# Kernel tuning notes

Hardware: AMD Instinct MI355X
Metric: run time of the kernel (lower is better)

Reference implementation:

```python
import jax, jax.numpy as jnp
import numpy as np

B, N, C = 16, 3136, 384
H = W = 56
HEADS = 8
DH = C // HEADS
AG = 49          # agent_num
PS = 7           # pool size (sqrt(agent_num)); H % PS == 0 -> exact block mean
OUT = 1000
SCALE = DH ** -0.5


def setup_inputs() -> dict:
    key = jax.random.key(0)
    ks = jax.random.split(key, 16)
    f32 = jnp.float32

    def nrm(k, sh, s=0.02):
        return jax.random.normal(k, sh, f32) * s

    return dict(
        x=jax.random.normal(ks[0], (B, N, C), f32),
        Wq=nrm(ks[1], (C, C)),
        Wkv=nrm(ks[2], (C, 2 * C)),
        an_bias=nrm(ks[3], (HEADS, AG, H, W)),
        na_bias=nrm(ks[4], (HEADS, AG, H, W)),
        ah_bias=nrm(ks[5], (1, HEADS, AG, H, 1)),
        aw_bias=nrm(ks[6], (1, HEADS, AG, 1, W)),
        ha_bias=nrm(ks[7], (1, HEADS, H, 1, AG)),
        wa_bias=nrm(ks[8], (1, HEADS, 1, W, AG)),
        dwc_w=nrm(ks[9], (C, 1, 3, 3), 0.1),   # depthwise 3x3, groups=C (OIHW, I=1)
        dwc_b=jnp.zeros((C,), f32),
        Wproj=nrm(ks[10], (C, C)),
        bproj=jnp.zeros((C,), f32),
        ln_g=jnp.ones((C,), f32),
        ln_b=jnp.zeros((C,), f32),
        W1=nrm(ks[11], (C, 2 * C)),
        b1=jnp.zeros((2 * C,), f32),
        W2=nrm(ks[12], (2 * C, OUT)),
        b2=jnp.zeros((OUT,), f32),
    )


def _layernorm(x, g, b, eps=1e-5):
    m = x.mean(-1, keepdims=True)
    v = ((x - m) ** 2).mean(-1, keepdims=True)
    return (x - m) * jax.lax.rsqrt(v + eps) * g + b


def reference(x, Wq, Wkv, an_bias, na_bias, ah_bias, aw_bias, ha_bias, wa_bias,
              dwc_w, dwc_b, Wproj, bproj, ln_g, ln_b, W1, b1, W2, b2):
    q = x @ Wq                                  # (B,N,C)
    kv = x @ Wkv                                # (B,N,2C)  (sr_ratio=1 path)
    k, v = kv[..., :C], kv[..., C:]

    # agent tokens: AdaptiveAvgPool2d(7) on (B,C,56,56) == exact 8x8 block mean
    agent = q.reshape(B, PS, H // PS, PS, W // PS, C).mean((2, 4)).reshape(B, AG, C)

    qh = q.reshape(B, N, HEADS, DH).transpose(0, 2, 1, 3)      # (B,h,N,d)
    kh = k.reshape(B, N, HEADS, DH).transpose(0, 2, 1, 3)
    vh = v.reshape(B, N, HEADS, DH).transpose(0, 2, 1, 3)
    ah = agent.reshape(B, AG, HEADS, DH).transpose(0, 2, 1, 3)  # (B,h,AG,d)

    # stage 1: agent -> kv. bilinear interp to same size == identity (sr=1)
    pos_bias = an_bias.reshape(1, HEADS, AG, N) + (ah_bias + aw_bias).reshape(1, HEADS, AG, N)
    agent_attn = jax.nn.softmax(
        jnp.einsum('bhad,bhnd->bhan', ah * SCALE, kh) + pos_bias, axis=-1)
    agent_v = jnp.einsum('bhan,bhnd->bhad', agent_attn, vh)     # (B,h,AG,d)

    # stage 2: query -> agent
    agent_bias = (na_bias.reshape(1, HEADS, AG, N).transpose(0, 1, 3, 2)
                  + (ha_bias + wa_bias).reshape(1, HEADS, N, AG))
    q_attn = jax.nn.softmax(
        jnp.einsum('bhnd,bhad->bhna', qh * SCALE, ah) + agent_bias, axis=-1)
    out = jnp.einsum('bhna,bhad->bhnd', q_attn, agent_v)
    out = out.transpose(0, 2, 1, 3).reshape(B, N, C)

    # depthwise conv residual on v (sr=1 -> no interpolation)
    v_img = v.reshape(B, H, W, C).transpose(0, 3, 1, 2)          # (B,C,H,W)
    dwc = jax.lax.conv_general_dilated(
        v_img, dwc_w, (1, 1), 'SAME', feature_group_count=C,
        dimension_numbers=('NCHW', 'OIHW', 'NCHW')) + dwc_b[None, :, None, None]
    out = out + dwc.transpose(0, 2, 3, 1).reshape(B, N, C)

    out = out @ Wproj + bproj
    pooled = out.mean(axis=1)                   # adaptive_avg_pool2d to 1x1
    h1 = _layernorm(pooled, ln_g, ln_b)
    h1 = jax.nn.gelu(h1 @ W1 + b1, approximate=False)
    return h1 @ W2 + b2                         # (B, OUT)
```

## Files before the change

kernel.cpp:

```cpp
#include <hip/hip_runtime.h>
#include <hip/hip_bf16.h>
#include <math.h>

#define BB 16
#define NN 3136
#define CC 384
#define HDS 8
#define DHH 48
#define AGG 49
#define HI 56
#define WI 56
#define OUTD 1000
#define SCALE_F 0.14433756729740643f
#define QKVC 1152

typedef __attribute__((ext_vector_type(8))) short short8;
typedef __attribute__((ext_vector_type(4))) float f32x4;

__device__ __forceinline__ float bf2f(unsigned short u) {
  union { unsigned u32; float f; } x;
  x.u32 = ((unsigned)u) << 16;
  return x.f;
}
__device__ __forceinline__ unsigned short f2bf(float f) {
  union { float f; unsigned u; } x;
  x.f = f;
  unsigned u = x.u;
  unsigned r = (u + 0x7fffu + ((u >> 16) & 1u)) >> 16;
  return (unsigned short)r;
}

__device__ __forceinline__ size_t xp_off(int gb, int ks, int j, int lane) {
  return ((((size_t)gb * 12 + ks) * 4 + j) * 64 + lane) * 8;
}
__device__ __forceinline__ size_t wp_off(int blk, int ks, int i, int lane) {
  return ((((size_t)blk * 12 + ks) * 4 + i) * 64 + lane) * 8;
}
__device__ __forceinline__ size_t vtp_off(int bh, int chunk, int half, int ntd, int lane) {
  return ((((size_t)bh * 49 + chunk) * 2 + half) * 3 + ntd) * 512 + lane * 8;
}

__global__ __launch_bounds__(256) void pack_x(const float* __restrict__ x,
                                              unsigned short* __restrict__ xp) {
  __shared__ unsigned short xlds[64 * 200];
  int gb = blockIdx.x;
  int tid = threadIdx.x;
  int lane = tid & 63, wv = tid >> 6;
  int lo = lane & 15, g = lane >> 4;
  int tok0 = gb * 64;

  for (int kh = 0; kh < 2; kh++) {
    if (kh) __syncthreads();
#pragma unroll
    for (int it = 0; it < 12; it++) {
      int idx = tid + it * 256;
      int tok = idx / 48, k4 = idx % 48;
      float4 f = *(const float4*)&x[(size_t)(tok0 + tok) * 384 + kh * 192 + k4 * 4];
      uint2 o;
      o.x = (unsigned)f2bf(f.x) | ((unsigned)f2bf(f.y) << 16);
      o.y = (unsigned)f2bf(f.z) | ((unsigned)f2bf(f.w) << 16);
      *(uint2*)&xlds[tok * 200 + k4 * 4] = o;
    }
    __syncthreads();
    for (int p = wv; p < 24; p += 4) {
      int ks = p >> 2, j = p & 3;
      uint4 v = *(const uint4*)&xlds[(j * 16 + lo) * 200 + ks * 32 + g * 8];
      *(uint4*)&xp[xp_off(gb, kh * 6 + ks, j, lane)] = v;
    }
  }
}

__global__ __launch_bounds__(256) void pack_w(const float* __restrict__ Wq,
                                              const float* __restrict__ Wkv,
                                              unsigned short* __restrict__ wp) {
  __shared__ unsigned short wlds[64 * 392];
  int blk = blockIdx.x;
  int col0 = blk * 64;
  const float* src;
  int ncol, nloc;
  if (col0 < 384) { src = Wq; ncol = 384; nloc = col0; }
  else            { src = Wkv; ncol = 768; nloc = col0 - 384; }
  int tid = threadIdx.x;
  int lane = tid & 63, wv = tid >> 6;
  int lo = lane & 15, g = lane >> 4;

#pragma unroll
  for (int it = 0; it < 96; it++) {
    int idx = tid + it * 256;
    int k = idx >> 6, col = idx & 63;
    wlds[col * 392 + k] = f2bf(src[(size_t)k * ncol + nloc + col]);
  }
  __syncthreads();
  for (int p = wv; p < 48; p += 4) {
    int ks = p >> 2, i = p & 3;
    uint4 v = *(const uint4*)&wlds[(i * 16 + lo) * 392 + ks * 32 + g * 8];
    *(uint4*)&wp[wp_off(blk, ks, i, lane)] = v;
  }
}

__global__ __launch_bounds__(256, 2) void gemm_v4(const unsigned short* __restrict__ xp,
                                                  const unsigned short* __restrict__ wp,
                                                  unsigned short* __restrict__ Y) {
  const int tid = threadIdx.x;
  const int lane = tid & 63;
  const int wave = tid >> 6;
  const int lo = lane & 15, g = lane >> 4;
  const int wt2 = wave & 1;
  const int wn2 = wave >> 1;

  int wg = blockIdx.x;
  int xcd = wg & 7, idx8 = wg >> 3;
  const int sq = 220, sr = 4;
  int l = (xcd < sr ? xcd * (sq + 1) : sr * (sq + 1) + (xcd - sr) * sq) + idx8;
  int bx = l % 9, by = l / 9;

  const int gbb = by * 4 + wt2 * 2;
  const unsigned short* wbase = wp + wp_off(bx * 2 + wn2, 0, 0, lane);
  const unsigned short* xbase0 = xp + xp_off(gbb + 0, 0, 0, lane);
  const unsigned short* xbase1 = xp + xp_off(gbb + 1, 0, 0, lane);

  f32x4 acc[4][8];
#pragma unroll
  for (int i = 0; i < 4; i++)
#pragma unroll
    for (int jj = 0; jj < 8; jj++) acc[i][jj] = (f32x4)0.f;

  short8 wfA[4], xfA[8], wfB[4], xfB[8];

  auto loadF = [&](short8* wf, short8* xf, int ks) {
    const unsigned short* wptr = wbase + (size_t)ks * 2048;
#pragma unroll
    for (int i = 0; i < 4; i++) wf[i] = *(const short8*)(wptr + i * 512);
    const unsigned short* x0 = xbase0 + (size_t)ks * 2048;
    const unsigned short* x1 = xbase1 + (size_t)ks * 2048;
#pragma unroll
    for (int j = 0; j < 4; j++) {
      xf[j] = *(const short8*)(x0 + j * 512);
      xf[4 + j] = *(const short8*)(x1 + j * 512);
    }
  };
  auto mfmaF = [&](short8* wf, short8* xf) {
    __builtin_amdgcn_s_setprio(1);
#pragma unroll
    for (int i = 0; i < 4; i++)
#pragma unroll
      for (int jj = 0; jj < 8; jj++)
        acc[i][jj] = __builtin_amdgcn_mfma_f32_16x16x32_bf16(wf[i], xf[jj], acc[i][jj], 0, 0, 0);
    __builtin_amdgcn_s_setprio(0);
  };

  loadF(wfA, xfA, 0);
#pragma unroll
  for (int kp = 0; kp < 6; kp++) {
    loadF(wfB, xfB, 2 * kp + 1);
    mfmaF(wfA, xfA);
    if (kp < 5) loadF(wfA, xfA, 2 * kp + 2);
    mfmaF(wfB, xfB);
  }

#pragma unroll
  for (int jj = 0; jj < 8; jj++) {
    int token = (gbb + (jj >> 2)) * 64 + (jj & 3) * 16 + lo;
#pragma unroll
    for (int i = 0; i < 4; i++) {
      int ncol = bx * 128 + wn2 * 64 + i * 16 + g * 4;
      uint2 o;
      o.x = (unsigned)f2bf(acc[i][jj][0]) | ((unsigned)f2bf(acc[i][jj][1]) << 16);
      o.y = (unsigned)f2bf(acc[i][jj][2]) | ((unsigned)f2bf(acc[i][jj][3]) << 16);
      *(uint2*)&Y[(size_t)token * QKVC + ncol] = o;
    }
  }
}

__global__ __launch_bounds__(256) void make_cbias2(
    const float* __restrict__ na, const float* __restrict__ ha,
    const float* __restrict__ wa, const float* __restrict__ an,
    const float* __restrict__ ah, const float* __restrict__ aw,
    unsigned short* __restrict__ cb1t, unsigned short* __restrict__ cb2t) {
  int blk = blockIdx.x;
  int h = blk / 49, nc = blk % 49;
  int a = threadIdx.x & 63, sub = threadIdx.x >> 6;
  int ac = a < AGG ? a : AGG - 1;
  bool va = a < AGG;
  size_t hab = (size_t)h * AGG + ac;
#pragma unroll
  for (int i = 0; i < 16; i++) {
    int n = nc * 64 + i * 4 + sub;
    int r = n / WI, c = n % WI;
    float v1 = na[hab * NN + n] + ha[(h * HI + r) * AGG + ac] + wa[(h * WI + c) * AGG + ac];
    float v2 = an[hab * NN + n] + ah[hab * HI + r] + aw[hab * WI + c];
    size_t ob = ((size_t)h * NN + n) * 52;
    if (a < 52) {
      cb1t[ob + a] = va ? f2bf(v1) : (unsigned short)0;
      cb2t[ob + a] = va ? f2bf(v2) : (unsigned short)0;
    }
  }
}

#define VSTR 396
__global__ __launch_bounds__(256) void pack_vt(const unsigned short* __restrict__ qkv,
                                               unsigned short* __restrict__ vtp) {
  __shared__ unsigned short vlds[64 * VSTR];
  int blk = blockIdx.x;
  int b = blk / 49, chunk = blk % 49;
  int tid = threadIdx.x, lane = tid & 63, wv = tid >> 6;
  int lo = lane & 15, g = lane >> 4;

#pragma unroll
  for (int it = 0; it < 12; it++) {
    int idx = tid + it * 256;
    int t = idx / 48, d8 = idx % 48;
    short8 v = *(const short8*)&qkv[((size_t)b * NN + chunk * 64 + t) * QKVC + 768 + d8 * 8];
    *(uint2*)&vlds[t * VSTR + d8 * 8] = ((uint2*)&v)[0];
    *(uint2*)&vlds[t * VSTR + d8 * 8 + 4] = ((uint2*)&v)[1];
  }
  __syncthreads();
  int bh8 = b * 8;
#pragma unroll
  for (int p = 0; p < 12; p++) {
    int fid = wv * 12 + p;
    int h = fid / 6, rem = fid % 6, half = rem / 3, ntd = rem % 3;
    unsigned short tmp[8];
#pragma unroll
    for (int e = 0; e < 8; e++)
      tmp[e] = vlds[(half * 32 + g * 8 + e) * VSTR + h * 48 + ntd * 16 + lo];
    *(uint4*)&vtp[vtp_off(bh8 + h, chunk, half, ntd, lane)] = *(uint4*)tmp;
  }
}

__global__ __launch_bounds__(384) void pool_agent(const unsigned short* __restrict__ qkv,
                                                  unsigned short* __restrict__ agbf) {
  int blk = blockIdx.x;
  int b = blk / AGG, a = blk % AGG;
  int p1 = a / 7, p2 = a % 7;
  int c = threadIdx.x;
  float s = 0.f;
#pragma unroll
  for (int i = 0; i < 8; i++)
#pragma unroll
    for (int j = 0; j < 8; j++) {
      int n = (p1 * 8 + i) * WI + (p2 * 8 + j);
      s += bf2f(qkv[((size_t)b * NN + n) * QKVC + c]);
    }
  agbf[(size_t)blk * CC + c] = f2bf(s * (1.f / 64.f));
}

__global__ __launch_bounds__(256) void agent_attn_v5(
    const unsigned short* __restrict__ qkv, const unsigned short* __restrict__ agbf,
    const unsigned short* __restrict__ cb2t, const unsigned short* __restrict__ vtp,
    float* __restrict__ lpart, float* __restrict__ avpart) {
  int z = blockIdx.x;
  int s = z & 3;
  int h = (z >> 2) & 7;
  int b = z >> 5;
  int tid = threadIdx.x, lane = tid & 63, wv = tid >> 6;
  int lo = lane & 15, g = lane >> 4;
  int slot = s * 4 + wv;
  int cstart = (slot == 0) ? 0 : 3 * slot + 1;
  int ccount = (slot == 0) ? 4 : 3;
  int bh = b * 8 + h;

  __shared__ __align__(16) unsigned short pT[4][64 * 72];
  __shared__ float ldsAV[AGG * 48];
  __shared__ float ldsL[AGG];
  for (int i = tid; i < AGG * 48; i += 256) ldsAV[i] = 0.f;
  if (tid < AGG) ldsL[tid] = 0.f;
  __syncthreads();

  short8 af0[4], af1[4];
#pragma unroll
  for (int mt = 0; mt < 4; mt++) {
    int a = mt * 16 + lo;
    int ac = a < AGG ? a : AGG - 1;
    const unsigned short* p = agbf + ((size_t)b * AGG + ac) * CC + h * 48;
    af0[mt] = *(const short8*)(p + g * 8);
    if (g < 2) af1[mt] = *(const short8*)(p + 32 + g * 8);
    else { short8 zz = {0, 0, 0, 0, 0, 0, 0, 0}; af1[mt] = zz; }
  }

  f32x4 acc2[4][3];
#pragma unroll
  for (int mt = 0; mt < 4; mt++)
#pragma unroll
    for (int ntd = 0; ntd < 3; ntd++) acc2[mt][ntd] = (f32x4)0.f;
  float lacc[4][4];
#pragma unroll
  for (int mt = 0; mt < 4; mt++)
#pragma unroll
    for (int r = 0; r < 4; r++) lacc[mt][r] = 0.f;

  for (int ci = 0; ci < ccount; ci++) {
    int chunk = cstart + ci;
    int nb = chunk * 64;

    short8 kf0[4], kf1[4];
#pragma unroll
    for (int nt = 0; nt < 4; nt++) {
      const unsigned short* kp = qkv + ((size_t)b * NN + nb + nt * 16 + lo) * QKVC + 384 + h * 48;
      kf0[nt] = *(const short8*)(kp + g * 8);
      if (g < 2) kf1[nt] = *(const short8*)(kp + 32 + g * 8);
      else { short8 zz = {0, 0, 0, 0, 0, 0, 0, 0}; kf1[nt] = zz; }
    }
    ushort4 cbv[4][4];
#pragma unroll
    for (int mt = 0; mt < 4; mt++)
#pragma unroll
      for (int nt = 0; nt < 4; nt++)
        cbv[mt][nt] = *(const ushort4*)&cb2t[((size_t)h * NN + nb + nt * 16 + lo) * 52 + mt * 16 + g * 4];
    short8 vb0[3], vb1[3];
#pragma unroll
    for (int ntd = 0; ntd < 3; ntd++) {
      vb0[ntd] = *(const short8*)&vtp[vtp_off(bh, chunk, 0, ntd, lane)];
      vb1[ntd] = *(const short8*)&vtp[vtp_off(bh, chunk, 1, ntd, lane)];
    }

    f32x4 acc[4][4];
#pragma unroll
    for (int mt = 0; mt < 4; mt++)
#pragma unroll
      for (int nt = 0; nt < 4; nt++) acc[mt][nt] = (f32x4)0.f;
#pragma unroll
    for (int mt = 0; mt < 4; mt++)
#pragma unroll
      for (int nt = 0; nt < 4; nt++) {
        acc[mt][nt] = __builtin_amdgcn_mfma_f32_16x16x32_bf16(af0[mt], kf0[nt], acc[mt][nt], 0, 0, 0);
        acc[mt][nt] = __builtin_amdgcn_mfma_f32_16x16x32_bf16(af1[mt], kf1[nt], acc[mt][nt], 0, 0, 0);
      }

#pragma unroll
    for (int mt = 0; mt < 4; mt++)
#pragma unroll
      for (int nt = 0; nt < 4; nt++) {
        unsigned short cb4[4] = {cbv[mt][nt].x, cbv[mt][nt].y, cbv[mt][nt].z, cbv[mt][nt].w};
#pragma unroll
        for (int r = 0; r < 4; r++) {
          int a = mt * 16 + g * 4 + r;
          float e = 0.f;
          if (a < AGG) e = __expf(acc[mt][nt][r] * SCALE_F + bf2f(cb4[r]));
          acc[mt][nt][r] = e;
        }
      }
#pragma unroll
    for (int mt = 0; mt < 4; mt++)
#pragma unroll
      for (int r = 0; r < 4; r++)
        lacc[mt][r] += acc[mt][0][r] + acc[mt][1][r] + acc[mt][2][r] + acc[mt][3][r];
#pragma unroll
    for (int mt = 0; mt < 4; mt++)
#pragma unroll
      for (int nt = 0; nt < 4; nt++)
#pragma unroll
        for (int r = 0; r < 4; r++) {
          int a = mt * 16 + g * 4 + r;
          int t = nt * 16 + lo;
          pT[wv][a * 72 + t] = f2bf(acc[mt][nt][r]);
        }

    short8 pa0[4], pa1[4];
#pragma unroll
    for (int mt = 0; mt < 4; mt++) {
      const unsigned short* p = &pT[wv][(mt * 16 + lo) * 72 + g * 8];
      pa0[mt] = *(const short8*)p;
      pa1[mt] = *(const short8*)(p + 32);
    }
#pragma unroll
    for (int mt = 0; mt < 4; mt++)
#pragma unroll
      for (int ntd = 0; ntd < 3; ntd++) {
        acc2[mt][ntd] = __builtin_amdgcn_mfma_f32_16x16x32_bf16(pa0[mt], vb0[ntd], acc2[mt][ntd], 0, 0, 0);
        acc2[mt][ntd] = __builtin_amdgcn_mfma_f32_16x16x32_bf16(pa1[mt], vb1[ntd], acc2[mt][ntd], 0, 0, 0);
      }
  }

#pragma unroll
  for (int mt = 0; mt < 4; mt++)
#pragma unroll
    for (int r = 0; r < 4; r++) {
      float v = lacc[mt][r];
      v += __shfl_xor(v, 1); v += __shfl_xor(v, 2);
      v += __shfl_xor(v, 4); v += __shfl_xor(v, 8);
      if (lo == 0) {
        int a = mt * 16 + g * 4 + r;
        if (a < AGG) atomicAdd(&ldsL[a], v);
      }
    }
#pragma unroll
  for (int mt = 0; mt < 4; mt++)
#pragma unroll
    for (int ntd = 0; ntd < 3; ntd++)
#pragma unroll
      for (int r = 0; r < 4; r++) {
        int a = mt * 16 + g * 4 + r;
        if (a < AGG) atomicAdd(&ldsAV[a * 48 + ntd * 16 + lo], acc2[mt][ntd][r]);
      }
  __syncthreads();
  size_t pbase = (size_t)bh * 4 + s;
  for (int i = tid; i < AGG * 48; i += 256) avpart[pbase * 2352 + i] = ldsAV[i];
  if (tid < AGG) lpart[pbase * AGG + tid] = ldsL[tid];
}

__global__ __launch_bounds__(256) void av_normalize3(const float* __restrict__ lpart,
                                                     const float* __restrict__ avpart,
                                                     unsigned short* __restrict__ avtp) {
  int bh = blockIdx.x;
  int tid = threadIdx.x;
  __shared__ float linv[AGG];
  if (tid < AGG) {
    float l = 0.f;
#pragma unroll
    for (int s = 0; s < 4; s++) l += lpart[((size_t)bh * 4 + s) * AGG + tid];
    linv[tid] = 1.f / l;
  }
  __syncthreads();
  for (int idx = tid; idx < 48 * 64; idx += 256) {
    int d = idx >> 6, a = idx & 63;
    unsigned short o = 0;
    if (a < AGG) {
      float v = 0.f;
#pragma unroll
      for (int s = 0; s < 4; s++) v += avpart[((size_t)bh * 4 + s) * 2352 + a * 48 + d];
      o = f2bf(v * linv[a]);
    }
    avtp[(size_t)bh * 3072 + d * 64 + a] = o;
  }
}

__global__ __launch_bounds__(256) void q_attn_v5(
    const unsigned short* __restrict__ qkv, const unsigned short* __restrict__ agbf,
    const unsigned short* __restrict__ avtp, const unsigned short* __restrict__ cb1t,
    float* __restrict__ opart) {
  int z = blockIdx.x;
  int s = z & 3;
  int h = (z >> 2) & 7;
  int b = z >> 5;
  int tid = threadIdx.x, lane = tid & 63, wv = tid >> 6;
  int lo = lane & 15, g = lane >> 4;
  int slot = s * 4 + wv;
  int cstart = (slot == 0) ? 0 : 3 * slot + 1;
  int ccount = (slot == 0) ? 4 : 3;
  int bh = b * 8 + h;

  __shared__ __align__(16) unsigned short pT[4][64 * 72];
  __shared__ float ldsO[48];
  if (tid < 48) ldsO[tid] = 0.f;
  __syncthreads();

  short8 af0[4], af1[4];
#pragma unroll
  for (int mt = 0; mt < 4; mt++) {
    int a = mt * 16 + lo;
    int ac = a < AGG ? a : AGG - 1;
    const unsigned short* p = agbf + ((size_t)b * AGG + ac) * CC + h * 48;
    af0[mt] = *(const short8*)(p + g * 8);
    if (g < 2) af1[mt] = *(const short8*)(p + 32 + g * 8);
    else { short8 zz = {0, 0, 0, 0, 0, 0, 0, 0}; af1[mt] = zz; }
  }
  short8 vf0[3], vf1[3];
#pragma unroll
  for (int mtd = 0; mtd < 3; mtd++) {
    size_t base = ((size_t)bh * 48 + mtd * 16 + lo) * 64;
    vf0[mtd] = *(const short8*)&avtp[base + g * 8];
    vf1[mtd] = *(const short8*)&avtp[base + 32 + g * 8];
  }

  f32x4 acc2[3][4];
#pragma unroll
  for (int mtd = 0; mtd < 3; mtd++)
#pragma unroll
    for (int nt = 0; nt < 4; nt++) acc2[mtd][nt] = (f32x4)0.f;

  for (int ci = 0; ci < ccount; ci++) {
    int nb = (cstart + ci) * 64;

    short8 qf0[4], qf1[4];
#pragma unroll
    for (int nt = 0; nt < 4; nt++) {
      const unsigned short* qp = qkv + ((size_t)b * NN + nb + nt * 16 + lo) * QKVC + h * 48;
      qf0[nt] = *(const short8*)(qp + g * 8);
      if (g < 2) qf1[nt] = *(const short8*)(qp + 32 + g * 8);
      else { short8 zz = {0, 0, 0, 0, 0, 0, 0, 0}; qf1[nt] = zz; }
    }
    ushort4 cbv[4][4];
#pragma unroll
    for (int mt = 0; mt < 4; mt++)
#pragma unroll
      for (int nt = 0; nt < 4; nt++)
        cbv[mt][nt] = *(const ushort4*)&cb1t[((size_t)h * NN + nb + nt * 16 + lo) * 52 + mt * 16 + g * 4];

    f32x4 acc[4][4];
#pragma unroll
    for (int mt = 0; mt < 4; mt++)
#pragma unroll
      for (int nt = 0; nt < 4; nt++) acc[mt][nt] = (f32x4)0.f;
#pragma unroll
    for (int mt = 0; mt < 4; mt++)
#pragma unroll
      for (int nt = 0; nt < 4; nt++) {
        acc[mt][nt] = __builtin_amdgcn_mfma_f32_16x16x32_bf16(af0[mt], qf0[nt], acc[mt][nt], 0, 0, 0);
        acc[mt][nt] = __builtin_amdgcn_mfma_f32_16x16x32_bf16(af1[mt], qf1[nt], acc[mt][nt], 0, 0, 0);
      }

#pragma unroll
    for (int nt = 0; nt < 4; nt++) {
      float lsum = 0.f;
#pragma unroll
      for (int mt = 0; mt < 4; mt++) {
        unsigned short cb4[4] = {cbv[mt][nt].x, cbv[mt][nt].y, cbv[mt][nt].z, cbv[mt][nt].w};
#pragma unroll
        for (int r = 0; r < 4; r++) {
          int a = mt * 16 + g * 4 + r;
          float e = 0.f;
          if (a < AGG) e = __expf(acc[mt][nt][r] * SCALE_F + bf2f(cb4[r]));
          acc[mt][nt][r] = e;
          lsum += e;
        }
      }
      lsum += __shfl_xor(lsum, 16);
      lsum += __shfl_xor(lsum, 32);
      float inv = 1.f / lsum;
      int t = nt * 16 + lo;
#pragma unroll
      for (int mt = 0; mt < 4; mt++)
#pragma unroll
        for (int rp = 0; rp < 2; rp++) {
          unsigned u0 = f2bf(acc[mt][nt][rp * 2] * inv);
          unsigned u1 = f2bf(acc[mt][nt][rp * 2 + 1] * inv);
          int a = mt * 16 + g * 4 + rp * 2;
          *(unsigned*)&pT[wv][t * 72 + a] = u0 | (u1 << 16);
        }
    }

    short8 pf0[4], pf1[4];
#pragma unroll
    for (int nt = 0; nt < 4; nt++) {
      const unsigned short* p = &pT[wv][(nt * 16 + lo) * 72 + g * 8];
      pf0[nt] = *(const short8*)p;
      pf1[nt] = *(const short8*)(p + 32);
    }
#pragma unroll
    for (int mtd = 0; mtd < 3; mtd++)
#pragma unroll
      for (int nt = 0; nt < 4; nt++) {
        acc2[mtd][nt] = __builtin_amdgcn_mfma_f32_16x16x32_bf16(vf0[mtd], pf0[nt], acc2[mtd][nt], 0, 0, 0);
        acc2[mtd][nt] = __builtin_amdgcn_mfma_f32_16x16x32_bf16(vf1[mtd], pf1[nt], acc2[mtd][nt], 0, 0, 0);
      }
  }

#pragma unroll
  for (int mtd = 0; mtd < 3; mtd++)
#pragma unroll
    for (int r = 0; r < 4; r++) {
      float v = acc2[mtd][0][r] + acc2[mtd][1][r] + acc2[mtd][2][r] + acc2[mtd][3][r];
      v += __shfl_xor(v, 1); v += __shfl_xor(v, 2);
      v += __shfl_xor(v, 4); v += __shfl_xor(v, 8);
      if (lo == 0) atomicAdd(&ldsO[mtd * 16 + g * 4 + r], v);
    }
  __syncthreads();
  if (tid < 48) opart[((size_t)bh * 4 + s) * 48 + tid] = ldsO[tid];
}

__global__ __launch_bounds__(384) void dwc_rows(const unsigned short* __restrict__ qkv,
                                                float* __restrict__ rowsum,
                                                float* __restrict__ edge0,
                                                float* __restrict__ edge1) {
  int z = blockIdx.x;
  int b = z / HI, r = z % HI;
  int c = threadIdx.x;
  const unsigned short* base = qkv + ((size_t)b * NN + (size_t)r * WI) * QKVC + 768 + c;
  float s = 0.f, e0 = 0.f, e1 = 0.f;
  for (int w = 0; w < WI; w++) {
    float v = bf2f(base[(size_t)w * QKVC]);
    s += v;
    if (w == 0) e0 = v;
    if (w == WI - 1) e1 = v;
  }
  rowsum[(size_t)z * CC + c] = s;
  edge0[(size_t)z * CC + c] = e0;
  edge1[(size_t)z * CC + c] = e1;
}

__global__ __launch_bounds__(384) void dwc_combine1(const float* __restrict__ rowsum,
                                                    const float* __restrict__ edge0,
                                                    const float* __restrict__ edge1,
                                                    float* __restrict__ dpart,
                                                    float* __restrict__ dedge) {
  int z = blockIdx.x;
  int b = z / 7, rc = z % 7;
  int c = threadIdx.x;
  float T = 0.f, C0 = 0.f, C55 = 0.f;
#pragma unroll
  for (int rr = 0; rr < 8; rr++) {
    int r = rc * 8 + rr;
    size_t idx = ((size_t)(b * HI + r)) * CC + c;
    float rs = rowsum[idx], a0 = edge0[idx], a1 = edge1[idx];
    T += rs; C0 += a0; C55 += a1;
    if (r == 0) {
      dedge[((size_t)b * 6 + 0) * CC + c] = rs;
      dedge[((size_t)b * 6 + 1) * CC + c] = a0;
      dedge[((size_t)b * 6 + 2) * CC + c] = a1;
    }
    if (r == HI - 1) {
      dedge[((size_t)b * 6 + 3) * CC + c] = rs;
      dedge[((size_t)b * 6 + 4) * CC + c] = a0;
      dedge[((size_t)b * 6 + 5) * CC + c] = a1;
    }
  }
  size_t pb = ((size_t)(b * 7 + rc) * 3) * CC + c;
  dpart[pb] = T;
  dpart[pb + CC] = C0;
  dpart[pb + 2 * CC] = C55;
}

__global__ __launch_bounds__(384) void head_pre(const float* __restrict__ dpart,
                                                const float* __restrict__ dedge,
                                                const float* __restrict__ opart,
                                                const float* __restrict__ w,
                                                const float* __restrict__ dwc_b,
                                                float* __restrict__ pre) {
  int b = blockIdx.x;
  int k = threadIdx.x;
  float T = 0.f, C0 = 0.f, C55 = 0.f;
#pragma unroll
  for (int rc = 0; rc < 7; rc++) {
    size_t pb = ((size_t)(b * 7 + rc) * 3) * CC + k;
    T += dpart[pb];
    C0 += dpart[pb + CC];
    C55 += dpart[pb + 2 * CC];
  }
  float R0 = dedge[((size_t)b * 6 + 0) * CC + k];
  float v00 = dedge[((size_t)b * 6 + 1) * CC + k];
  float v0W = dedge[((size_t)b * 6 + 2) * CC + k];
  float R55 = dedge[((size_t)b * 6 + 3) * CC + k];
  float vH0 = dedge[((size_t)b * 6 + 4) * CC + k];
  float vHW = dedge[((size_t)b * 6 + 5) * CC + k];
  float dwcsum = 0.f;
#pragma unroll
  for (int i = 0; i < 3; i++) {
    int di = i - 1;
#pragma unroll
    for (int j = 0; j < 3; j++) {
      int dj = j - 1;
      float S = T;
      if (di == 1) S -= R0; else if (di == -1) S -= R55;
      if (dj == 1) S -= C0; else if (dj == -1) S -= C55;
      if (di != 0 && dj != 0)
        S += (di == 1) ? ((dj == 1) ? v00 : v0W) : ((dj == 1) ? vH0 : vHW);
      dwcsum += w[k * 9 + i * 3 + j] * S;
    }
  }
  int hh = k / 48, dd = k % 48;
  size_t obase = ((size_t)(b * 8 + hh) * 4) * 48;
  float attn = 0.f;
#pragma unroll
  for (int s = 0; s < 4; s++) attn += opart[obase + s * 48 + dd];
  pre[(size_t)b * CC + k] = (dwcsum + attn) * (1.f / (float)NN) + dwc_b[k];
}

__global__ __launch_bounds__(256) void head_proj_part(
    const float* __restrict__ pre, const float* __restrict__ Wproj,
    float* __restrict__ pjpart) {
  int w = blockIdx.x * 4 + (threadIdx.x >> 6);
  int lane = threadIdx.x & 63;
  int b = w / 36, rem = w % 36;
  int oc = rem / 6, kc = rem % 6;
  int o = oc * 64 + lane;
  const float* pb = pre + (size_t)b * CC + kc * 64;
  const float* wp2 = Wproj + (size_t)(kc * 64) * CC + o;
  float s = 0.f;
#pragma unroll 16
  for (int k = 0; k < 64; k++) s += pb[k] * wp2[(size_t)k * CC];
  pjpart[((size_t)(b * 6 + kc)) * CC + o] = s;
}

__global__ __launch_bounds__(384) void head_ln6(const float* __restrict__ pjpart,
                                                const float* __restrict__ bproj,
                                                const float* __restrict__ ln_g,
                                                const float* __restrict__ ln_b,
                                                float* __restrict__ h0) {
  int b = blockIdx.x;
  int tid = threadIdx.x;
  __shared__ float red[8];
  float v = bproj[tid];
#pragma unroll
  for (int kc = 0; kc < 6; kc++) v += pjpart[((size_t)(b * 6 + kc)) * CC + tid];
  float m;
  {
    float s = v;
#pragma unroll
    for (int o = 32; o > 0; o >>= 1) s += __shfl_down(s, o);
    if ((tid & 63) == 0) red[tid >> 6] = s;
    __syncthreads();
    if (tid == 0) {
      float t = 0.f;
      for (int i = 0; i < 6; i++) t += red[i];
      red[6] = t * (1.f / (float)CC);
    }
    __syncthreads();
    m = red[6];
  }
  float dv = v - m;
  __syncthreads();
  float var;
  {
    float s = dv * dv;
#pragma unroll
    for (int o = 32; o > 0; o >>= 1) s += __shfl_down(s, o);
    if ((tid & 63) == 0) red[tid >> 6] = s;
    __syncthreads();
    if (tid == 0) {
      float t = 0.f;
      for (int i = 0; i < 6; i++) t += red[i];
      red[7] = t * (1.f / (float)CC);
    }
    __syncthreads();
    var = red[7];
  }
  h0[(size_t)b * CC + tid] = dv * rsqrtf(var + 1e-5f) * ln_g[tid] + ln_b[tid];
}

__global__ __launch_bounds__(256) void head_mlp1_part(
    const float* __restrict__ h0, const float* __restrict__ W1,
    float* __restrict__ h1part) {
  int w = blockIdx.x * 4 + (threadIdx.x >> 6);
  int lane = threadIdx.x & 63;
  int b = w / 72, rem = w % 72;
  int oc = rem / 6, kc = rem % 6;
  int o = oc * 64 + lane;
  const float* hb = h0 + (size_t)b * CC + kc * 64;
  const float* wp2 = W1 + (size_t)(kc * 64) * (2 * CC) + o;
  float s = 0.f;
#pragma unroll 16
  for (int k = 0; k < 64; k++) s += hb[k] * wp2[(size_t)k * (2 * CC)];
  h1part[((size_t)(b * 6 + kc)) * (2 * CC) + o] = s;
}

__global__ __launch_bounds__(256) void head_mlp1_red(const float* __restrict__ h1part,
                                                     const float* __restrict__ b1,
                                                     float* __restrict__ h1) {
  int b = blockIdx.x;
  for (int o = threadIdx.x; o < 2 * CC; o += 256) {
    float s = b1[o];
#pragma unroll
    for (int kc = 0; kc < 6; kc++) s += h1part[((size_t)(b * 6 + kc)) * (2 * CC) + o];
    h1[(size_t)b * (2 * CC) + o] = 0.5f * s * (1.f + erff(s * 0.70710678118654752f));
  }
}

__global__ __launch_bounds__(256) void head_mlp2_part(
    const float* __restrict__ h1, const float* __restrict__ W2,
    float* __restrict__ o2part) {
  int w = blockIdx.x * 4 + (threadIdx.x >> 6);
  int lane = threadIdx.x & 63;
  int b = w / 192, rem = w % 192;
  int oc = rem / 12, kc = rem % 12;
  int o = oc * 64 + lane;
  int ocl = o < OUTD ? o : OUTD - 1;
  const float* hb = h1 + (size_t)b * (2 * CC) + kc * 64;
  const float* wp2 = W2 + (size_t)(kc * 64) * OUTD + ocl;
  float s = 0.f;
#pragma unroll 16
  for (int k = 0; k < 64; k++) s += hb[k] * wp2[(size_t)k * OUTD];
  o2part[((size_t)(b * 12 + kc)) * 1024 + o] = s;
}

__global__ __launch_bounds__(256) void head_out(const float* __restrict__ o2part,
                                                const float* __restrict__ b2,
                                                float* __restrict__ out) {
  int b = blockIdx.x;
  for (int o = threadIdx.x; o < OUTD; o += 256) {
    float s = b2[o];
#pragma unroll
    for (int kc = 0; kc < 12; kc++) s += o2part[((size_t)(b * 12 + kc)) * 1024 + o];
    out[(size_t)b * OUTD + o] = s;
  }
}

extern "C" void kernel_launch(void* const* d_in, const int* in_sizes, int n_in,
                              void* d_out, int out_size, void* d_ws,
                              size_t ws_size, hipStream_t stream) {
  const float* x = (const float*)d_in[0];
  const float* Wq = (const float*)d_in[1];
  const float* Wkv = (const float*)d_in[2];
  const float* an_bias = (const float*)d_in[3];
  const float* na_bias = (const float*)d_in[4];
  const float* ah_bias = (const float*)d_in[5];
  const float* aw_bias = (const float*)d_in[6];
  const float* ha_bias = (const float*)d_in[7];
  const float* wa_bias = (const float*)d_in[8];
  const float* dwc_w = (const float*)d_in[9];
  const float* dwc_b = (const float*)d_in[10];
  const float* Wproj = (const float*)d_in[11];
  const float* bproj = (const float*)d_in[12];
  const float* ln_g = (const float*)d_in[13];
  const float* ln_b = (const float*)d_in[14];
  const float* W1 = (const float*)d_in[15];
  const float* b1 = (const float*)d_in[16];
  const float* W2 = (const float*)d_in[17];
  const float* b2 = (const float*)d_in[18];
  float* out = (float*)d_out;

  const size_t M = (size_t)BB * NN;
  char* wsp = (char*)d_ws;
  unsigned short* xp = (unsigned short*)wsp;
  unsigned short* vtp = xp;
  wsp += M * CC * 2;
  unsigned short* wpb = (unsigned short*)wsp;   wsp += (size_t)QKVC * CC * 2;
  unsigned short* qkv = (unsigned short*)wsp;   wsp += M * QKVC * 2;
  unsigned short* agbf = (unsigned short*)wsp;  wsp += (size_t)784 * CC * 2;
  unsigned short* cb1t = (unsigned short*)wsp;  wsp += (size_t)HDS * NN * 52 * 2;
  unsigned short* cb2t = (unsigned short*)wsp;  wsp += (size_t)HDS * NN * 52 * 2;
  float* lpart = (float*)wsp;                   wsp += (size_t)128 * 4 * AGG * 4;
  float* avpart = (float*)wsp;                  wsp += (size_t)128 * 4 * 2352 * 4;
  unsigned short* avtp = (unsigned short*)wsp;  wsp += (size_t)128 * 3072 * 2;
  float* opart = (float*)wsp;                   wsp += (size_t)128 * 4 * 48 * 4;
  float* rowsum = (float*)wsp;                  wsp += (size_t)BB * HI * CC * 4;
  float* edge0 = (float*)wsp;                   wsp += (size_t)BB * HI * CC * 4;
  float* edge1 = (float*)wsp;                   wsp += (size_t)BB * HI * CC * 4;
  float* dpart = (float*)wsp;                   wsp += (size_t)BB * 7 * 3 * CC * 4;
  float* dedge = (float*)wsp;                   wsp += (size_t)BB * 6 * CC * 4;
  float* pre = (float*)wsp;                     wsp += (size_t)BB * CC * 4;
  float* pjpart = (float*)wsp;                  wsp += (size_t)BB * 6 * CC * 4;
  float* h0b = (float*)wsp;                     wsp += (size_t)BB * CC * 4;
  float* h1part = (float*)wsp;                  wsp += (size_t)BB * 6 * 2 * CC * 4;
  float* h1b = (float*)wsp;                     wsp += (size_t)BB * 2 * CC * 4;
  float* o2part = (float*)wsp;                  wsp += (size_t)BB * 12 * 1024 * 4;

  dim3 blk256(256);
  hipLaunchKernelGGL(pack_x, dim3(784), blk256, 0, stream, x, xp);
  hipLaunchKernelGGL(pack_w, dim3(18), blk256, 0, stream, Wq, Wkv, wpb);
  hipLaunchKernelGGL(make_cbias2, dim3(HDS * 49), blk256, 0, stream, na_bias,
                     ha_bias, wa_bias, an_bias, ah_bias, aw_bias, cb1t, cb2t);
  hipLaunchKernelGGL(gemm_v4, dim3(1764), blk256, 0, stream, xp, wpb, qkv);
  hipLaunchKernelGGL(pack_vt, dim3(BB * 49), blk256, 0, stream, qkv, vtp);
  hipLaunchKernelGGL(pool_agent, dim3(BB * AGG), dim3(384), 0, stream, qkv, agbf);
  hipLaunchKernelGGL(agent_attn_v5, dim3(BB * HDS * 4), blk256, 0, stream,
                     qkv, agbf, cb2t, vtp, lpart, avpart);
  hipLaunchKernelGGL(av_normalize3, dim3(BB * HDS), blk256, 0, stream, lpart,
                     avpart, avtp);
  hipLaunchKernelGGL(q_attn_v5, dim3(BB * HDS * 4), blk256, 0, stream, qkv,
                     agbf, avtp, cb1t, opart);
  hipLaunchKernelGGL(dwc_rows, dim3(BB * HI), dim3(384), 0, stream, qkv, rowsum,
                     edge0, edge1);
  hipLaunchKernelGGL(dwc_combine1, dim3(BB * 7), dim3(384), 0, stream, rowsum,
                     edge0, edge1, dpart, dedge);
  hipLaunchKernelGGL(head_pre, dim3(BB), dim3(384), 0, stream, dpart, dedge,
                     opart, dwc_w, dwc_b, pre);
  hipLaunchKernelGGL(head_proj_part, dim3(144), blk256, 0, stream, pre, Wproj, pjpart);
  hipLaunchKernelGGL(head_ln6, dim3(BB), dim3(384), 0, stream, pjpart, bproj,
                     ln_g, ln_b, h0b);
  hipLaunchKernelGGL(head_mlp1_part, dim3(288), blk256, 0, stream, h0b, W1, h1part);
  hipLaunchKernelGGL(head_mlp1_red, dim3(BB), blk256, 0, stream, h1part, b1, h1b);
  hipLaunchKernelGGL(head_mlp2_part, dim3(768), blk256, 0, stream, h1b, W2, o2part);
  hipLaunchKernelGGL(head_out, dim3(BB), blk256, 0, stream, o2part, b2, out);
}
```

Before: 268.4 us.

## Double-buffer K/Q fragment loads and write per-wave partials instead of LDS atomics

Both attention kernels now prefetch the next chunk's K (or Q) fragments into a second register set while the current chunk is computed, which hides global load latency. The shared-memory atomic reductions and their barriers are removed. Each wave now writes its own partial sums to global memory (16 slots per batch-head instead of 4), and the normalize and head kernels sum over 16 partials. This costs more registers, 4x larger partial buffers and more global traffic in the reduction kernels.

```diff
diff --git a/kernel.cpp b/kernel.cpp
--- a/kernel.cpp
+++ b/kernel.cpp
@@ -245,7 +245,7 @@
   agbf[(size_t)blk * CC + c] = f2bf(s * (1.f / 64.f));
 }
 
-__global__ __launch_bounds__(256) void agent_attn_v5(
+__global__ __launch_bounds__(256) void agent_attn_v7(
     const unsigned short* __restrict__ qkv, const unsigned short* __restrict__ agbf,
     const unsigned short* __restrict__ cb2t, const unsigned short* __restrict__ vtp,
     float* __restrict__ lpart, float* __restrict__ avpart) {
@@ -261,11 +261,6 @@
   int bh = b * 8 + h;
 
   __shared__ __align__(16) unsigned short pT[4][64 * 72];
-  __shared__ float ldsAV[AGG * 48];
-  __shared__ float ldsL[AGG];
-  for (int i = tid; i < AGG * 48; i += 256) ldsAV[i] = 0.f;
-  if (tid < AGG) ldsL[tid] = 0.f;
-  __syncthreads();
 
   short8 af0[4], af1[4];
 #pragma unroll
@@ -289,18 +284,19 @@
 #pragma unroll
     for (int r = 0; r < 4; r++) lacc[mt][r] = 0.f;
 
-  for (int ci = 0; ci < ccount; ci++) {
-    int chunk = cstart + ci;
+  auto loadK = [&](short8* k0, short8* k1, int chunk) {
     int nb = chunk * 64;
-
-    short8 kf0[4], kf1[4];
 #pragma unroll
     for (int nt = 0; nt < 4; nt++) {
       const unsigned short* kp = qkv + ((size_t)b * NN + nb + nt * 16 + lo) * QKVC + 384 + h * 48;
-      kf0[nt] = *(const short8*)(kp + g * 8);
-      if (g < 2) kf1[nt] = *(const short8*)(kp + 32 + g * 8);
-      else { short8 zz = {0, 0, 0, 0, 0, 0, 0, 0}; kf1[nt] = zz; }
-    }
+      k0[nt] = *(const short8*)(kp + g * 8);
+      if (g < 2) k1[nt] = *(const short8*)(kp + 32 + g * 8);
+      else { short8 zz = {0, 0, 0, 0, 0, 0, 0, 0}; k1[nt] = zz; }
+    }
+  };
+
+  auto body = [&](short8* k0, short8* k1, int chunk) {
+    int nb = chunk * 64;
     ushort4 cbv[4][4];
 #pragma unroll
     for (int mt = 0; mt < 4; mt++)
@@ -323,8 +319,8 @@
     for (int mt = 0; mt < 4; mt++)
 #pragma unroll
       for (int nt = 0; nt < 4; nt++) {
-        acc[mt][nt] = __builtin_amdgcn_mfma_f32_16x16x32_bf16(af0[mt], kf0[nt], acc[mt][nt], 0, 0, 0);
-        acc[mt][nt] = __builtin_amdgcn_mfma_f32_16x16x32_bf16(af1[mt], kf1[nt], acc[mt][nt], 0, 0, 0);
+        acc[mt][nt] = __builtin_amdgcn_mfma_f32_16x16x32_bf16(af0[mt], k0[nt], acc[mt][nt], 0, 0, 0);
+        acc[mt][nt] = __builtin_amdgcn_mfma_f32_16x16x32_bf16(af1[mt], k1[nt], acc[mt][nt], 0, 0, 0);
       }
 
 #pragma unroll
@@ -370,8 +366,21 @@
         acc2[mt][ntd] = __builtin_amdgcn_mfma_f32_16x16x32_bf16(pa0[mt], vb0[ntd], acc2[mt][ntd], 0, 0, 0);
         acc2[mt][ntd] = __builtin_amdgcn_mfma_f32_16x16x32_bf16(pa1[mt], vb1[ntd], acc2[mt][ntd], 0, 0, 0);
       }
-  }
-
+  };
+
+  short8 kA0[4], kA1[4], kB0[4], kB1[4];
+  loadK(kA0, kA1, cstart);
+  int ci = 0;
+  while (true) {
+    if (ci + 1 < ccount) loadK(kB0, kB1, cstart + ci + 1);
+    body(kA0, kA1, cstart + ci);
+    if (++ci >= ccount) break;
+    if (ci + 1 < ccount) loadK(kA0, kA1, cstart + ci + 1);
+    body(kB0, kB1, cstart + ci);
+    if (++ci >= ccount) break;
+  }
+
+  size_t pbase = (size_t)bh * 16 + slot;
 #pragma unroll
   for (int mt = 0; mt < 4; mt++)
 #pragma unroll
@@ -379,10 +388,8 @@
       float v = lacc[mt][r];
       v += __shfl_xor(v, 1); v += __shfl_xor(v, 2);
       v += __shfl_xor(v, 4); v += __shfl_xor(v, 8);
-      if (lo == 0) {
-        int a = mt * 16 + g * 4 + r;
-        if (a < AGG) atomicAdd(&ldsL[a], v);
-      }
+      int a = mt * 16 + g * 4 + r;
+      if (lo == 0 && a < AGG) lpart[pbase * AGG + a] = v;
     }
 #pragma unroll
   for (int mt = 0; mt < 4; mt++)
@@ -391,12 +398,9 @@
 #pragma unroll
       for (int r = 0; r < 4; r++) {
         int a = mt * 16 + g * 4 + r;
-        if (a < AGG) atomicAdd(&ldsAV[a * 48 + ntd * 16 + lo], acc2[mt][ntd][r]);
+        if (a < AGG)
+          avpart[pbase * 2352 + a * 48 + ntd * 16 + lo] = acc2[mt][ntd][r];
       }
-  __syncthreads();
-  size_t pbase = (size_t)bh * 4 + s;
-  for (int i = tid; i < AGG * 48; i += 256) avpart[pbase * 2352 + i] = ldsAV[i];
-  if (tid < AGG) lpart[pbase * AGG + tid] = ldsL[tid];
 }
 
 __global__ __launch_bounds__(256) void av_normalize3(const float* __restrict__ lpart,
@@ -408,7 +412,7 @@
   if (tid < AGG) {
     float l = 0.f;
 #pragma unroll
-    for (int s = 0; s < 4; s++) l += lpart[((size_t)bh * 4 + s) * AGG + tid];
+    for (int s = 0; s < 16; s++) l += lpart[((size_t)bh * 16 + s) * AGG + tid];
     linv[tid] = 1.f / l;
   }
   __syncthreads();
@@ -418,14 +422,14 @@
     if (a < AGG) {
       float v = 0.f;
 #pragma unroll
-      for (int s = 0; s < 4; s++) v += avpart[((size_t)bh * 4 + s) * 2352 + a * 48 + d];
+      for (int s = 0; s < 16; s++) v += avpart[((size_t)bh * 16 + s) * 2352 + a * 48 + d];
       o = f2bf(v * linv[a]);
     }
     avtp[(size_t)bh * 3072 + d * 64 + a] = o;
   }
 }
 
-__global__ __launch_bounds__(256) void q_attn_v5(
+__global__ __launch_bounds__(256) void q_attn_v7(
     const unsigned short* __restrict__ qkv, const unsigned short* __restrict__ agbf,
     const unsigned short* __restrict__ avtp, const unsigned short* __restrict__ cb1t,
     float* __restrict__ opart) {
@@ -441,9 +445,6 @@
   int bh = b * 8 + h;
 
   __shared__ __align__(16) unsigned short pT[4][64 * 72];
-  __shared__ float ldsO[48];
-  if (tid < 48) ldsO[tid] = 0.f;
-  __syncthreads();
 
   short8 af0[4], af1[4];
 #pragma unroll
@@ -469,17 +470,19 @@
 #pragma unroll
     for (int nt = 0; nt < 4; nt++) acc2[mtd][nt] = (f32x4)0.f;
 
-  for (int ci = 0; ci < ccount; ci++) {
-    int nb = (cstart + ci) * 64;
-
-    short8 qf0[4], qf1[4];
+  auto loadQ = [&](short8* q0, short8* q1, int chunk) {
+    int nb = chunk * 64;
 #pragma unroll
     for (int nt = 0; nt < 4; nt++) {
       const unsigned short* qp = qkv + ((size_t)b * NN + nb + nt * 16 + lo) * QKVC + h * 48;
-      qf0[nt] = *(const short8*)(qp + g * 8);
-      if (g < 2) qf1[nt] = *(const short8*)(qp + 32 + g * 8);
-      else { short8 zz = {0, 0, 0, 0, 0, 0, 0, 0}; qf1[nt] = zz; }
-    }
+      q0[nt] = *(const short8*)(qp + g * 8);
+      if (g < 2) q1[nt] = *(const short8*)(qp + 32 + g * 8);
+      else { short8 zz = {0, 0, 0, 0, 0, 0, 0, 0}; q1[nt] = zz; }
+    }
+  };
+
+  auto body = [&](short8* q0, short8* q1, int chunk) {
+    int nb = chunk * 64;
     ushort4 cbv[4][4];
 #pragma unroll
     for (int mt = 0; mt < 4; mt++)
@@ -496,8 +499,8 @@
     for (int mt = 0; mt < 4; mt++)
 #pragma unroll
       for (int nt = 0; nt < 4; nt++) {
-        acc[mt][nt] = __builtin_amdgcn_mfma_f32_16x16x32_bf16(af0[mt], qf0[nt], acc[mt][nt], 0, 0, 0);
-        acc[mt][nt] = __builtin_amdgcn_mfma_f32_16x16x32_bf16(af1[mt], qf1[nt], acc[mt][nt], 0, 0, 0);
+        acc[mt][nt] = __builtin_amdgcn_mfma_f32_16x16x32_bf16(af0[mt], q0[nt], acc[mt][nt], 0, 0, 0);
+        acc[mt][nt] = __builtin_amdgcn_mfma_f32_16x16x32_bf16(af1[mt], q1[nt], acc[mt][nt], 0, 0, 0);
       }
 
 #pragma unroll
@@ -544,8 +547,21 @@
         acc2[mtd][nt] = __builtin_amdgcn_mfma_f32_16x16x32_bf16(vf0[mtd], pf0[nt], acc2[mtd][nt], 0, 0, 0);
         acc2[mtd][nt] = __builtin_amdgcn_mfma_f32_16x16x32_bf16(vf1[mtd], pf1[nt], acc2[mtd][nt], 0, 0, 0);
       }
-  }
-
+  };
+
+  short8 qA0[4], qA1[4], qB0[4], qB1[4];
+  loadQ(qA0, qA1, cstart);
+  int ci = 0;
+  while (true) {
+    if (ci + 1 < ccount) loadQ(qB0, qB1, cstart + ci + 1);
+    body(qA0, qA1, cstart + ci);
+    if (++ci >= ccount) break;
+    if (ci + 1 < ccount) loadQ(qA0, qA1, cstart + ci + 1);
+    body(qB0, qB1, cstart + ci);
+    if (++ci >= ccount) break;
+  }
+
+  size_t pbase = (size_t)bh * 16 + slot;
 #pragma unroll
   for (int mtd = 0; mtd < 3; mtd++)
 #pragma unroll
@@ -553,10 +569,8 @@
       float v = acc2[mtd][0][r] + acc2[mtd][1][r] + acc2[mtd][2][r] + acc2[mtd][3][r];
       v += __shfl_xor(v, 1); v += __shfl_xor(v, 2);
       v += __shfl_xor(v, 4); v += __shfl_xor(v, 8);
-      if (lo == 0) atomicAdd(&ldsO[mtd * 16 + g * 4 + r], v);
-    }
-  __syncthreads();
-  if (tid < 48) opart[((size_t)bh * 4 + s) * 48 + tid] = ldsO[tid];
+      if (lo == 0) opart[pbase * 48 + mtd * 16 + g * 4 + r] = v;
+    }
 }
 
 __global__ __launch_bounds__(384) void dwc_rows(const unsigned short* __restrict__ qkv,
@@ -649,10 +663,10 @@
     }
   }
   int hh = k / 48, dd = k % 48;
-  size_t obase = ((size_t)(b * 8 + hh) * 4) * 48;
+  size_t obase = ((size_t)(b * 8 + hh) * 16) * 48;
   float attn = 0.f;
 #pragma unroll
-  for (int s = 0; s < 4; s++) attn += opart[obase + s * 48 + dd];
+  for (int s = 0; s < 16; s++) attn += opart[obase + s * 48 + dd];
   pre[(size_t)b * CC + k] = (dwcsum + attn) * (1.f / (float)NN) + dwc_b[k];
 }
 
@@ -809,10 +823,10 @@
   unsigned short* agbf = (unsigned short*)wsp;  wsp += (size_t)784 * CC * 2;
   unsigned short* cb1t = (unsigned short*)wsp;  wsp += (size_t)HDS * NN * 52 * 2;
   unsigned short* cb2t = (unsigned short*)wsp;  wsp += (size_t)HDS * NN * 52 * 2;
-  float* lpart = (float*)wsp;                   wsp += (size_t)128 * 4 * AGG * 4;
-  float* avpart = (float*)wsp;                  wsp += (size_t)128 * 4 * 2352 * 4;
+  float* lpart = (float*)wsp;                   wsp += (size_t)128 * 16 * AGG * 4;
+  float* avpart = (float*)wsp;                  wsp += (size_t)128 * 16 * 2352 * 4;
   unsigned short* avtp = (unsigned short*)wsp;  wsp += (size_t)128 * 3072 * 2;
-  float* opart = (float*)wsp;                   wsp += (size_t)128 * 4 * 48 * 4;
+  float* opart = (float*)wsp;                   wsp += (size_t)128 * 16 * 48 * 4;
   float* rowsum = (float*)wsp;                  wsp += (size_t)BB * HI * CC * 4;
   float* edge0 = (float*)wsp;                   wsp += (size_t)BB * HI * CC * 4;
   float* edge1 = (float*)wsp;                   wsp += (size_t)BB * HI * CC * 4;
@@ -833,11 +847,11 @@
   hipLaunchKernelGGL(gemm_v4, dim3(1764), blk256, 0, stream, xp, wpb, qkv);
   hipLaunchKernelGGL(pack_vt, dim3(BB * 49), blk256, 0, stream, qkv, vtp);
   hipLaunchKernelGGL(pool_agent, dim3(BB * AGG), dim3(384), 0, stream, qkv, agbf);
-  hipLaunchKernelGGL(agent_attn_v5, dim3(BB * HDS * 4), blk256, 0, stream,
+  hipLaunchKernelGGL(agent_attn_v7, dim3(BB * HDS * 4), blk256, 0, stream,
                      qkv, agbf, cb2t, vtp, lpart, avpart);
   hipLaunchKernelGGL(av_normalize3, dim3(BB * HDS), blk256, 0, stream, lpart,
                      avpart, avtp);
-  hipLaunchKernelGGL(q_attn_v5, dim3(BB * HDS * 4), blk256, 0, stream, qkv,
+  hipLaunchKernelGGL(q_attn_v7, dim3(BB * HDS * 4), blk256, 0, stream, qkv,
                      agbf, avtp, cb1t, opart);
   hipLaunchKernelGGL(dwc_rows, dim3(BB * HI), dim3(384), 0, stream, qkv, rowsum,
                      edge0, edge1);
```

After: 273.3 us. About the same (+1.8%).

## Sum query-agent attention over tokens before multiplying by agent values

Applied to the files above, without the earlier changes.

Because only the token-mean of the attention output is needed, the query-side kernel now accumulates per-agent softmax probability sums instead of running a second MFMA against agent_v. The agent_v product moves into head_pre as a small 49-term dot product using fp32 agent_v, and the bf16 transposed agent_v packing is dropped. This removes the LDS staging, the bf16 conversion and the second matmul from the hot kernel. In exchange, head_pre does a little more work and reads more partials (16 slots per head).

```diff
diff --git a/kernel.cpp b/kernel.cpp
--- a/kernel.cpp
+++ b/kernel.cpp
@@ -399,9 +399,9 @@
   if (tid < AGG) lpart[pbase * AGG + tid] = ldsL[tid];
 }
 
-__global__ __launch_bounds__(256) void av_normalize3(const float* __restrict__ lpart,
+__global__ __launch_bounds__(256) void av_normalize4(const float* __restrict__ lpart,
                                                      const float* __restrict__ avpart,
-                                                     unsigned short* __restrict__ avtp) {
+                                                     float* __restrict__ av) {
   int bh = blockIdx.x;
   int tid = threadIdx.x;
   __shared__ float linv[AGG];
@@ -412,23 +412,18 @@
     linv[tid] = 1.f / l;
   }
   __syncthreads();
-  for (int idx = tid; idx < 48 * 64; idx += 256) {
-    int d = idx >> 6, a = idx & 63;
-    unsigned short o = 0;
-    if (a < AGG) {
-      float v = 0.f;
-#pragma unroll
-      for (int s = 0; s < 4; s++) v += avpart[((size_t)bh * 4 + s) * 2352 + a * 48 + d];
-      o = f2bf(v * linv[a]);
-    }
-    avtp[(size_t)bh * 3072 + d * 64 + a] = o;
-  }
-}
-
-__global__ __launch_bounds__(256) void q_attn_v5(
+  for (int idx = tid; idx < AGG * 48; idx += 256) {
+    int a = idx / 48;
+    float v = 0.f;
+#pragma unroll
+    for (int s = 0; s < 4; s++) v += avpart[((size_t)bh * 4 + s) * 2352 + idx];
+    av[(size_t)bh * 2352 + idx] = v * linv[a];
+  }
+}
+
+__global__ __launch_bounds__(256) void q_attn_v9(
     const unsigned short* __restrict__ qkv, const unsigned short* __restrict__ agbf,
-    const unsigned short* __restrict__ avtp, const unsigned short* __restrict__ cb1t,
-    float* __restrict__ opart) {
+    const unsigned short* __restrict__ cb1t, float* __restrict__ opart) {
   int z = blockIdx.x;
   int s = z & 3;
   int h = (z >> 2) & 7;
@@ -440,11 +435,6 @@
   int ccount = (slot == 0) ? 4 : 3;
   int bh = b * 8 + h;
 
-  __shared__ __align__(16) unsigned short pT[4][64 * 72];
-  __shared__ float ldsO[48];
-  if (tid < 48) ldsO[tid] = 0.f;
-  __syncthreads();
-
   short8 af0[4], af1[4];
 #pragma unroll
   for (int mt = 0; mt < 4; mt++) {
@@ -455,19 +445,12 @@
     if (g < 2) af1[mt] = *(const short8*)(p + 32 + g * 8);
     else { short8 zz = {0, 0, 0, 0, 0, 0, 0, 0}; af1[mt] = zz; }
   }
-  short8 vf0[3], vf1[3];
-#pragma unroll
-  for (int mtd = 0; mtd < 3; mtd++) {
-    size_t base = ((size_t)bh * 48 + mtd * 16 + lo) * 64;
-    vf0[mtd] = *(const short8*)&avtp[base + g * 8];
-    vf1[mtd] = *(const short8*)&avtp[base + 32 + g * 8];
-  }
-
-  f32x4 acc2[3][4];
-#pragma unroll
-  for (int mtd = 0; mtd < 3; mtd++)
-#pragma unroll
-    for (int nt = 0; nt < 4; nt++) acc2[mtd][nt] = (f32x4)0.f;
+
+  float psum[4][4];
+#pragma unroll
+  for (int mt = 0; mt < 4; mt++)
+#pragma unroll
+    for (int r = 0; r < 4; r++) psum[mt][r] = 0.f;
 
   for (int ci = 0; ci < ccount; ci++) {
     int nb = (cstart + ci) * 64;
@@ -518,45 +501,25 @@
       lsum += __shfl_xor(lsum, 16);
       lsum += __shfl_xor(lsum, 32);
       float inv = 1.f / lsum;
-      int t = nt * 16 + lo;
 #pragma unroll
       for (int mt = 0; mt < 4; mt++)
 #pragma unroll
-        for (int rp = 0; rp < 2; rp++) {
-          unsigned u0 = f2bf(acc[mt][nt][rp * 2] * inv);
-          unsigned u1 = f2bf(acc[mt][nt][rp * 2 + 1] * inv);
-          int a = mt * 16 + g * 4 + rp * 2;
-          *(unsigned*)&pT[wv][t * 72 + a] = u0 | (u1 << 16);
-        }
-    }
-
-    short8 pf0[4], pf1[4];
-#pragma unroll
-    for (int nt = 0; nt < 4; nt++) {
-      const unsigned short* p = &pT[wv][(nt * 16 + lo) * 72 + g * 8];
-      pf0[nt] = *(const short8*)p;
-      pf1[nt] = *(const short8*)(p + 32);
-    }
-#pragma unroll
-    for (int mtd = 0; mtd < 3; mtd++)
-#pragma unroll
-      for (int nt = 0; nt < 4; nt++) {
-        acc2[mtd][nt] = __builtin_amdgcn_mfma_f32_16x16x32_bf16(vf0[mtd], pf0[nt], acc2[mtd][nt], 0, 0, 0);
-        acc2[mtd][nt] = __builtin_amdgcn_mfma_f32_16x16x32_bf16(vf1[mtd], pf1[nt], acc2[mtd][nt], 0, 0, 0);
-      }
-  }
-
-#pragma unroll
-  for (int mtd = 0; mtd < 3; mtd++)
+        for (int r = 0; r < 4; r++)
+          psum[mt][r] += acc[mt][nt][r] * inv;
+    }
+  }
+
+  size_t pbase = (size_t)bh * 16 + slot;
+#pragma unroll
+  for (int mt = 0; mt < 4; mt++)
 #pragma unroll
     for (int r = 0; r < 4; r++) {
-      float v = acc2[mtd][0][r] + acc2[mtd][1][r] + acc2[mtd][2][r] + acc2[mtd][3][r];
+      float v = psum[mt][r];
       v += __shfl_xor(v, 1); v += __shfl_xor(v, 2);
       v += __shfl_xor(v, 4); v += __shfl_xor(v, 8);
-      if (lo == 0) atomicAdd(&ldsO[mtd * 16 + g * 4 + r], v);
-    }
-  __syncthreads();
-  if (tid < 48) opart[((size_t)bh * 4 + s) * 48 + tid] = ldsO[tid];
+      int a = mt * 16 + g * 4 + r;
+      if (lo == 0 && a < AGG) opart[pbase * 52 + a] = v;
+    }
 }
 
 __global__ __launch_bounds__(384) void dwc_rows(const unsigned short* __restrict__ qkv,
@@ -614,11 +577,23 @@
 __global__ __launch_bounds__(384) void head_pre(const float* __restrict__ dpart,
                                                 const float* __restrict__ dedge,
                                                 const float* __restrict__ opart,
+                                                const float* __restrict__ av,
                                                 const float* __restrict__ w,
                                                 const float* __restrict__ dwc_b,
                                                 float* __restrict__ pre) {
   int b = blockIdx.x;
   int k = threadIdx.x;
+  __shared__ float psums[HDS][AGG];
+  for (int idx = k; idx < HDS * AGG; idx += 384) {
+    int hh = idx / AGG, a = idx % AGG;
+    float v = 0.f;
+#pragma unroll
+    for (int s = 0; s < 16; s++)
+      v += opart[(((size_t)(b * 8 + hh) * 16) + s) * 52 + a];
+    psums[hh][a] = v;
+  }
+  __syncthreads();
+
   float T = 0.f, C0 = 0.f, C55 = 0.f;
 #pragma unroll
   for (int rc = 0; rc < 7; rc++) {
@@ -648,11 +623,12 @@
       dwcsum += w[k * 9 + i * 3 + j] * S;
     }
   }
+
   int hh = k / 48, dd = k % 48;
-  size_t obase = ((size_t)(b * 8 + hh) * 4) * 48;
+  const float* avb = av + ((size_t)(b * 8 + hh)) * 2352 + dd;
   float attn = 0.f;
-#pragma unroll
-  for (int s = 0; s < 4; s++) attn += opart[obase + s * 48 + dd];
+#pragma unroll 7
+  for (int a = 0; a < AGG; a++) attn += psums[hh][a] * avb[(size_t)a * 48];
   pre[(size_t)b * CC + k] = (dwcsum + attn) * (1.f / (float)NN) + dwc_b[k];
 }
 
@@ -811,8 +787,8 @@
   unsigned short* cb2t = (unsigned short*)wsp;  wsp += (size_t)HDS * NN * 52 * 2;
   float* lpart = (float*)wsp;                   wsp += (size_t)128 * 4 * AGG * 4;
   float* avpart = (float*)wsp;                  wsp += (size_t)128 * 4 * 2352 * 4;
-  unsigned short* avtp = (unsigned short*)wsp;  wsp += (size_t)128 * 3072 * 2;
-  float* opart = (float*)wsp;                   wsp += (size_t)128 * 4 * 48 * 4;
+  float* av = (float*)wsp;                      wsp += (size_t)128 * 2352 * 4;
+  float* opart = (float*)wsp;                   wsp += (size_t)128 * 16 * 52 * 4;
   float* rowsum = (float*)wsp;                  wsp += (size_t)BB * HI * CC * 4;
   float* edge0 = (float*)wsp;                   wsp += (size_t)BB * HI * CC * 4;
   float* edge1 = (float*)wsp;                   wsp += (size_t)BB * HI * CC * 4;
@@ -835,16 +811,16 @@
   hipLaunchKernelGGL(pool_agent, dim3(BB * AGG), dim3(384), 0, stream, qkv, agbf);
   hipLaunchKernelGGL(agent_attn_v5, dim3(BB * HDS * 4), blk256, 0, stream,
                      qkv, agbf, cb2t, vtp, lpart, avpart);
-  hipLaunchKernelGGL(av_normalize3, dim3(BB * HDS), blk256, 0, stream, lpart,
-                     avpart, avtp);
-  hipLaunchKernelGGL(q_attn_v5, dim3(BB * HDS * 4), blk256, 0, stream, qkv,
-                     agbf, avtp, cb1t, opart);
+  hipLaunchKernelGGL(av_normalize4, dim3(BB * HDS), blk256, 0, stream, lpart,
+                     avpart, av);
+  hipLaunchKernelGGL(q_attn_v9, dim3(BB * HDS * 4), blk256, 0, stream, qkv,
+                     agbf, cb1t, opart);
   hipLaunchKernelGGL(dwc_rows, dim3(BB * HI), dim3(384), 0, stream, qkv, rowsum,
                      edge0, edge1);
   hipLaunchKernelGGL(dwc_combine1, dim3(BB * 7), dim3(384), 0, stream, rowsum,
                      edge0, edge1, dpart, dedge);
   hipLaunchKernelGGL(head_pre, dim3(BB), dim3(384), 0, stream, dpart, dedge,
-                     opart, dwc_w, dwc_b, pre);
+                     opart, av, dwc_w, dwc_b, pre);
   hipLaunchKernelGGL(head_proj_part, dim3(144), blk256, 0, stream, pre, Wproj, pjpart);
   hipLaunchKernelGGL(head_ln6, dim3(BB), dim3(384), 0, stream, pjpart, bproj,
                      ln_g, ln_b, h0b);
```

After: 265.8 us. About the same (-1.0%).
